# Kernel tuning notes

Hardware: AMD Instinct MI355X
Metric: run time of the kernel (lower is better)

## Reference

```python
import jax, jax.numpy as jnp
import numpy as np

BN_INV = 1.0 / np.float32(np.sqrt(1.0 + 1e-5))  # eval BN with running_mean=0, running_var=1


def _conv(x, w, stride):
    return jax.lax.conv_general_dilated(
        x, w, (stride, stride), [(1, 1), (1, 1)],
        dimension_numbers=('NCHW', 'OIHW', 'NCHW'))


def _se(x, w1, b1, w2, b2):
    # squeeze-excite: global avg pool -> fc -> relu -> fc -> sigmoid -> scale
    y = x.mean(axis=(2, 3))                       # (B, C)
    y = jax.nn.relu(y @ w1.T + b1)
    y = jax.nn.sigmoid(y @ w2.T + b2)
    return x * y[:, :, None, None]


def _squash(s):
    n2 = jnp.sum(s * s, axis=-1, keepdims=True)
    n = jnp.sqrt(n2)
    return s * (n2 / (1.0 + n2)) / (n + 1e-8)


def _block(x, cw, g, b, s1w, s1b, s2w, s2b, stride):
    h = _conv(x, cw, stride)
    h = h * (g * BN_INV)[None, :, None, None] + b[None, :, None, None]
    h = jax.nn.relu(h)
    return _se(h, s1w, s1b, s2w, s2b)


def setup_inputs() -> dict:
    key = jax.random.key(0)
    ks = jax.random.split(key, 32)
    rn = lambda i, shape, s=1.0: s * jax.random.normal(ks[i], shape, dtype=jnp.float32)
    d = {}
    d['x'] = rn(0, (64, 1, 128, 128))
    # feature extractor
    d['conv1_w'] = rn(1, (16, 1, 3, 3), 0.3)
    d['bn1_g'] = 1.0 + rn(2, (16,), 0.1)
    d['bn1_b'] = rn(3, (16,), 0.1)
    d['se1_w1'] = rn(4, (1, 16), 0.2); d['se1_b1'] = rn(5, (1,), 0.1)
    d['se1_w2'] = rn(6, (16, 1), 0.2); d['se1_b2'] = rn(7, (16,), 0.1)
    d['conv2_w'] = rn(8, (32, 16, 3, 3), 0.1)
    d['bn2_g'] = 1.0 + rn(9, (32,), 0.1)
    d['bn2_b'] = rn(10, (32,), 0.1)
    d['se2_w1'] = rn(11, (2, 32), 0.2); d['se2_b1'] = rn(12, (2,), 0.1)
    d['se2_w2'] = rn(13, (32, 2), 0.2); d['se2_b2'] = rn(14, (32,), 0.1)
    d['conv3_w'] = rn(15, (64, 32, 3, 3), 0.07)
    d['bn3_g'] = 1.0 + rn(16, (64,), 0.1)
    d['bn3_b'] = rn(17, (64,), 0.1)
    d['se3_w1'] = rn(18, (4, 64), 0.15); d['se3_b1'] = rn(19, (4,), 0.1)
    d['se3_w2'] = rn(20, (64, 4), 0.15); d['se3_b2'] = rn(21, (64,), 0.1)
    # primary capsules conv: 64 -> 8 caps * 8 dim = 64 channels, stride 2
    d['pc_w'] = rn(22, (64, 64, 3, 3), 0.05)
    d['pc_b'] = rn(23, (64,), 0.05)
    # digit capsule transform: (1, 2048, 3, 16, 8)
    d['W_digit'] = 0.01 * jax.random.normal(ks[24], (1, 2048, 3, 16, 8), dtype=jnp.float32)
    return d


def reference(x, conv1_w, bn1_g, bn1_b, se1_w1, se1_b1, se1_w2, se1_b2,
              conv2_w, bn2_g, bn2_b, se2_w1, se2_b1, se2_w2, se2_b2,
              conv3_w, bn3_g, bn3_b, se3_w1, se3_b1, se3_w2, se3_b2,
              pc_w, pc_b, W_digit):
    h = _block(x, conv1_w, bn1_g, bn1_b, se1_w1, se1_b1, se1_w2, se1_b2, 1)
    h = _block(h, conv2_w, bn2_g, bn2_b, se2_w1, se2_b1, se2_w2, se2_b2, 2)
    h = _block(h, conv3_w, bn3_g, bn3_b, se3_w1, se3_b1, se3_w2, se3_b2, 2)
    # primary capsules: conv -> (B, 8 caps, 8 dim, 16*16) -> (B, 2048, 8)
    u = _conv(h, pc_w, 2) + pc_b[None, :, None, None]     # (B, 64, 16, 16)
    B = u.shape[0]
    u = u.reshape(B, 8, 8, -1).transpose(0, 1, 3, 2).reshape(B, -1, 8)
    u = _squash(u)                                        # (B, 2048, 8)
    # u_hat[b,i,c,d] = sum_e W[0,i,c,d,e] * u[b,i,e]  (avoids torch's W.repeat)
    u_hat = jnp.einsum('icde,bie->bicd', W_digit[0], u)   # (B, 2048, 3, 16)
    b_ij = jnp.zeros((B, u_hat.shape[1], u_hat.shape[2], 1), u_hat.dtype)
    v_j = None
    for _ in range(3):  # fixed routing iterations
        c_ij = jax.nn.softmax(b_ij, axis=2)
        s_j = jnp.sum(c_ij * u_hat, axis=1, keepdims=True)  # (B,1,3,16)
        v_j = _squash(s_j)
        b_ij = b_ij + jnp.sum(u_hat * v_j, axis=-1, keepdims=True)
    v = v_j[:, 0]                                          # (B, 3, 16)
    return jnp.sqrt(jnp.sum(v * v, axis=-1))               # (B, 3) class lengths
```

## Files before the change

kernel.cpp:

```cpp
#include <hip/hip_runtime.h>
#include <math.h>

#define BN_INV_F 0.9999950000374997f

__device__ __forceinline__ void gload_lds4(const float* g, float* l) {
    __builtin_amdgcn_global_load_lds(
        (const __attribute__((address_space(1))) void*)g,
        (__attribute__((address_space(3))) void*)l, 4, 0, 0);
}
__device__ __forceinline__ void gload_lds16(const float* g, float* l) {
    __builtin_amdgcn_global_load_lds(
        (const __attribute__((address_space(1))) void*)g,
        (__attribute__((address_space(3))) void*)l, 16, 0, 0);
}

__global__ __launch_bounds__(256) void wtrans_all_k(
    const float* __restrict__ w1, const float* __restrict__ w2,
    const float* __restrict__ w3, const float* __restrict__ wp,
    float* __restrict__ w1t, float* __restrict__ w2t,
    float* __restrict__ w3t, float* __restrict__ wpt)
{
    int i = blockIdx.x * 256 + threadIdx.x;
    if (i < 144) {
        int co = i % 16, k = i / 16;
        w1t[i] = w1[co * 9 + k];
    } else if (i < 4752) {
        int t = i - 144;
        int co = t % 32, rk = t / 32, cin = rk / 9, k = rk % 9;
        w2t[t] = w2[(co * 16 + cin) * 9 + k];
    } else if (i < 23184) {
        int t = i - 4752;
        int co = t % 64, rk = t / 64, cin = rk / 9, k = rk % 9;
        w3t[t] = w3[(co * 32 + cin) * 9 + k];
    } else if (i < 60048) {
        int t = i - 23184;
        int co = t % 64, rk = t / 64, cin = rk / 9, k = rk % 9;
        wpt[t] = wp[(co * 64 + cin) * 9 + k];
    }
}

template <int CIN, int CINB, int COUT, int COB, int HIN, int HOUT, int STRIDE,
          int TW, int ROWS_T, int PPT, int CB, int NTHREADS,
          bool BN_RELU, bool SE_SUM, int HSE_IN, int KSPLIT>
__device__ __forceinline__ void conv_body(
    const float* __restrict__ in, const float* __restrict__ wt,
    const float* __restrict__ gamma, const float* __restrict__ beta,
    float* __restrict__ out, size_t pstride,
    float* __restrict__ se_sum, const float* __restrict__ se_sums_in,
    const float* __restrict__ se_w1, const float* __restrict__ se_b1,
    const float* __restrict__ se_w2, const float* __restrict__ se_b2,
    float inv_spatial)
{
    constexpr int WIN = HIN, WOUT = HOUT;
    constexpr int TH = ROWS_T * PPT;
    constexpr int IH_T = (TH - 1) * STRIDE + 3;
    constexpr int NW = NTHREADS / 64;
    constexpr int NCHUNK = CINB / CB;
    constexpr int SEGS = (WIN >= 64) ? (WIN / 64) : 1;
    constexpr int PAIRS = (IH_T + 1) / 2;
    constexpr int NG = COUT / COB;
    constexpr int IHW = IH_T * WIN;
    constexpr int CHUNK_BYTES = CB * IHW * 4;
    constexpr bool FAST16 = (CHUNK_BYTES % 1024) == 0;
    constexpr int NISS = CHUNK_BYTES / 1024;
    static_assert(NTHREADS == TW * ROWS_T, "geometry");
    static_assert(TW == WOUT, "tile must span full output width");
    static_assert(CINB % CB == 0, "chunking");
    static_assert(WIN % 64 == 0 || WIN == 32, "stage width");

    const int b = blockIdx.z;
    const int gy = blockIdx.y;
    const int ty = blockIdx.x;
    const int tid = threadIdx.x;
    const int wo = tid % TW;
    const int rg = tid / TW;
    const int g = gy % NG;
    const int kk = gy / NG;
    const int cin0 = kk * CINB;

    __shared__ float in_t[2][CB * IH_T * WIN];
    __shared__ float scl[CIN];
    __shared__ float gl[COB], bl[COB];
    __shared__ float red[NW][COB];
    __shared__ float hid[HSE_IN > 0 ? HSE_IN : 1];

    const float* inb = in + (size_t)b * CIN * HIN * WIN;
    const int gr0 = ty * TH * STRIDE - 1;
    const int wos = wo * STRIDE;
    const int wvid = tid >> 6, lane = tid & 63;
    const bool interior = (gr0 >= 0) && (gr0 + IH_T <= HIN);

    auto stage = [&](int c, int buf) {
        const int cb0 = cin0 + c * CB;
        float* bb = &in_t[buf][0];
        if (FAST16 && interior) {
            for (int i = wvid; i < NISS; i += NW) {
                int fe = i * 256 + lane * 4;
                int ci = fe / IHW;
                int rem = fe - ci * IHW;
                int lr = rem / WIN;
                int lc = rem - lr * WIN;
                const float* gsrc = inb + (size_t)(cb0 + ci) * (HIN * WIN)
                                  + (size_t)(gr0 + lr) * WIN + lc;
                gload_lds16(gsrc, bb + i * 256);
            }
        } else if (WIN >= 64) {
            for (int r = wvid; r < CB * IH_T; r += NW) {
                int ci = r / IH_T, lr = r - ci * IH_T;
                int gr = gr0 + lr;
                float* ldst = bb + (ci * IH_T + lr) * WIN;
                if (gr >= 0 && gr < HIN) {
                    const float* gsrc = inb + (size_t)(cb0 + ci) * HIN * WIN + (size_t)gr * WIN;
#pragma unroll
                    for (int s = 0; s < SEGS; ++s)
                        gload_lds4(gsrc + s * 64 + lane, ldst + s * 64);
                } else {
#pragma unroll
                    for (int s = 0; s < SEGS; ++s) ldst[s * 64 + lane] = 0.0f;
                }
            }
        } else {
            for (int pz = wvid; pz < CB * PAIRS; pz += NW) {
                int ci = pz / PAIRS, q = pz - ci * PAIRS;
                int lr0 = q * 2;
                int nr = (lr0 + 1 < IH_T) ? 2 : 1;
                int grr = gr0 + lr0;
                float* ldst = bb + (ci * IH_T + lr0) * WIN;
                if (nr == 2 && grr >= 0 && grr + 1 < HIN) {
                    const float* gsrc = inb + (size_t)(cb0 + ci) * HIN * WIN + (size_t)grr * WIN + lane;
                    gload_lds4(gsrc, ldst);
                } else {
                    for (int e = lane; e < nr * WIN; e += 64) {
                        int rr = e / WIN, cc = e - rr * WIN;
                        int gr = grr + rr;
                        ldst[e] = (gr >= 0 && gr < HIN)
                            ? inb[(size_t)(cb0 + ci) * HIN * WIN + (size_t)gr * WIN + cc] : 0.0f;
                    }
                }
            }
        }
    };

    stage(0, 0);

    if (HSE_IN > 0) {
        if (tid < HSE_IN) {
            float a = se_b1[tid];
            for (int c = 0; c < CIN; ++c)
                a = fmaf(se_sums_in[b * CIN + c] * inv_spatial, se_w1[tid * CIN + c], a);
            hid[tid] = fmaxf(a, 0.0f);
        }
        __syncthreads();
        if (tid < CIN) {
            float a = se_b2[tid];
            for (int h = 0; h < HSE_IN; ++h)
                a = fmaf(hid[h], se_w2[tid * HSE_IN + h], a);
            scl[tid] = 1.0f / (1.0f + expf(-a));
        }
    } else {
        for (int t = tid; t < CIN; t += NTHREADS) scl[t] = 1.0f;
    }
    if (tid < COB) {
        int co = g * COB + tid;
        if (BN_RELU) {
            gl[tid] = gamma[co] * BN_INV_F;
            bl[tid] = beta[co];
        } else {
            gl[tid] = (kk == 0) ? gamma[co] : 0.0f;
        }
    }

    float acc[PPT][COB];
#pragma unroll
    for (int p = 0; p < PPT; ++p)
#pragma unroll
        for (int co = 0; co < COB; ++co) acc[p][co] = 0.0f;

    int cur = 0;
    for (int c = 0; c < NCHUNK; ++c) {
        asm volatile("s_waitcnt vmcnt(0)" ::: "memory");
        __syncthreads();
        if (c + 1 < NCHUNK) stage(c + 1, cur ^ 1);

        const float* bb = &in_t[cur][0];
#pragma unroll
        for (int ci = 0; ci < CB; ++ci) {
            const int cw = cin0 + c * CB + ci;
            const float sc = scl[cw];
            const float* wtap = wt + (size_t)cw * 9 * COUT + g * COB;
            const float* bb_ci = bb + ci * IH_T * WIN;

            float iw[PPT][3][3];
#pragma unroll
            for (int p = 0; p < PPT; ++p) {
                const int r0 = (rg + p * ROWS_T) * STRIDE;
#pragma unroll
                for (int kh = 0; kh < 3; ++kh) {
                    const float* row = bb_ci + (r0 + kh) * WIN;
#pragma unroll
                    for (int kw = 0; kw < 3; ++kw) {
                        int wi = wos + kw - 1;
                        float v;
                        if (kw == 0) {
                            v = row[wi < 0 ? 0 : wi];
                            if (wi < 0) v = 0.0f;
                        } else if (STRIDE == 1 && kw == 2) {
                            v = row[wi >= WIN ? WIN - 1 : wi];
                            if (wi >= WIN) v = 0.0f;
                        } else {
                            v = row[wi];
                        }
                        iw[p][kh][kw] = v * sc;
                    }
                }
            }

#pragma unroll
            for (int kh = 0; kh < 3; ++kh) {
#pragma unroll
                for (int kw = 0; kw < 3; ++kw) {
                    const float* wrow = wtap + (kh * 3 + kw) * COUT;
#pragma unroll
                    for (int p = 0; p < PPT; ++p) {
                        const float v = iw[p][kh][kw];
#pragma unroll
                        for (int co = 0; co < COB; ++co)
                            acc[p][co] = fmaf(wrow[co], v, acc[p][co]);
                    }
                }
            }
        }
        cur ^= 1;
    }

    float tsum[COB];
#pragma unroll
    for (int co = 0; co < COB; ++co) tsum[co] = 0.0f;
    float* ob = out + (size_t)kk * pstride
              + ((size_t)b * COUT + (size_t)g * COB) * HOUT * WOUT;
#pragma unroll
    for (int p = 0; p < PPT; ++p) {
        const int ho = ty * TH + rg + p * ROWS_T;
#pragma unroll
        for (int co = 0; co < COB; ++co) {
            float v;
            if (BN_RELU)
                v = fmaxf(fmaf(acc[p][co], gl[co], bl[co]), 0.0f);
            else
                v = acc[p][co] + gl[co];
            ob[(size_t)co * HOUT * WOUT + ho * WOUT + wo] = v;
            tsum[co] += v;
        }
    }

    if (SE_SUM) {
#pragma unroll
        for (int co = 0; co < COB; ++co) {
            float v = tsum[co];
            for (int off = 32; off; off >>= 1) v += __shfl_down(v, off, 64);
            if (lane == 0) red[wvid][co] = v;
        }
        __syncthreads();
        if (tid < COB) {
            float v = 0.0f;
#pragma unroll
            for (int k = 0; k < NW; ++k) v += red[k][tid];
            atomicAdd(&se_sum[b * COUT + g * COB + tid], v);
        }
    }
}

#define CONV_ARGS \
    const float* __restrict__ in, const float* __restrict__ wt, \
    const float* __restrict__ gamma, const float* __restrict__ beta, \
    float* __restrict__ out, size_t pstride, float* __restrict__ se_sum, \
    const float* __restrict__ se_sums_in, \
    const float* __restrict__ se_w1, const float* __restrict__ se_b1, \
    const float* __restrict__ se_w2, const float* __restrict__ se_b2, \
    float inv_spatial
#define CONV_PASS in, wt, gamma, beta, out, pstride, se_sum, se_sums_in, \
    se_w1, se_b1, se_w2, se_b2, inv_spatial

__global__ __launch_bounds__(256) void conv1_k(CONV_ARGS) {
    conv_body<1, 1, 16, 16, 128, 128, 1, 128, 2, 2, 1, 256, true, true, 0, 1>(CONV_PASS);
}
__global__ __launch_bounds__(256) void conv2_k(CONV_ARGS) {
    conv_body<16, 16, 32, 32, 128, 64, 2, 64, 4, 1, 4, 256, true, true, 1, 1>(CONV_PASS);
}
__global__ __launch_bounds__(256) void conv3_k(CONV_ARGS) {
    conv_body<32, 16, 64, 32, 64, 32, 2, 32, 8, 1, 4, 256, false, false, 2, 2>(CONV_PASS);
}
__global__ __launch_bounds__(256) void pc_k(CONV_ARGS) {
    conv_body<64, 16, 64, 16, 32, 16, 2, 16, 16, 1, 4, 256, false, false, 4, 4>(CONV_PASS);
}

__global__ __launch_bounds__(256) void cb_k(const float* __restrict__ pA,
                                            const float* __restrict__ pB,
                                            const float* __restrict__ gamma,
                                            const float* __restrict__ beta,
                                            float* __restrict__ h3,
                                            float* __restrict__ s3)
{
    const int bc = blockIdx.x;
    const int c = bc & 63;
    const int tid = threadIdx.x;
    __shared__ float red[4];
    const size_t base = (size_t)bc * 1024;
    float4 a = ((const float4*)(pA + base))[tid];
    float4 d = ((const float4*)(pB + base))[tid];
    const float g = gamma[c] * BN_INV_F, be = beta[c];
    float4 v;
    v.x = fmaxf(fmaf(a.x + d.x, g, be), 0.0f);
    v.y = fmaxf(fmaf(a.y + d.y, g, be), 0.0f);
    v.z = fmaxf(fmaf(a.z + d.z, g, be), 0.0f);
    v.w = fmaxf(fmaf(a.w + d.w, g, be), 0.0f);
    ((float4*)(h3 + base))[tid] = v;
    float s = (v.x + v.y) + (v.z + v.w);
    for (int off = 32; off; off >>= 1) s += __shfl_down(s, off, 64);
    const int lane = tid & 63, wv = tid >> 6;
    if (lane == 0) red[wv] = s;
    __syncthreads();
    if (tid == 0) s3[bc] = (red[0] + red[1]) + (red[2] + red[3]);
}

__global__ __launch_bounds__(256) void squash_uhat_k(
    const float* __restrict__ up, size_t pstride,
    const float* __restrict__ W, float* __restrict__ u_hat)
{
    const int base = blockIdx.x * 256;
    const int tid = threadIdx.x;
    __shared__ float ush[256][8];

    {
        const int cap = base + tid;
        const int b = cap >> 11, i = cap & 2047;
        const int chi = i >> 8, spx = i & 255;
        const size_t off = ((size_t)(b * 64 + chi * 8)) * 256 + spx;
        float s[8];
        float n2 = 0.0f;
#pragma unroll
        for (int j = 0; j < 8; j++) {
            const size_t o = off + (size_t)j * 256;
            s[j] = (up[o] + up[o + pstride]) + (up[o + 2 * pstride] + up[o + 3 * pstride]);
            n2 = fmaf(s[j], s[j], n2);
        }
        const float n = sqrtf(n2);
        const float f = (n2 / (1.0f + n2)) / (n + 1e-8f);
#pragma unroll
        for (int j = 0; j < 8; j++) ush[tid][j] = s[j] * f;
    }
    __syncthreads();

    float* ob = u_hat + (size_t)base * 48;
#pragma unroll 4
    for (int k = 0; k < 48; ++k) {
        int o = tid + k * 256;
        int c = o / 48, cd = o % 48;
        int gi = (base + c) & 2047;
        const float* wp = W + (size_t)gi * 384 + cd * 8;
        float a = 0.0f;
#pragma unroll
        for (int e = 0; e < 8; e++) a = fmaf(wp[e], ush[c][e], a);
        ob[o] = a;
    }
}

template <int IT>
__global__ __launch_bounds__(256) void sweep_k(const float* __restrict__ u_hat,
                                               const float* __restrict__ s_hist,
                                               float* __restrict__ s_out)
{
    const int b = blockIdx.y;
    const int i = blockIdx.x * 256 + threadIdx.x;
    const int tid = threadIdx.x;
    __shared__ float vsh[IT > 0 ? IT : 1][48];
    __shared__ float fac[IT > 0 ? IT : 1][3];
    __shared__ float red[4][48];

    const float4* qp = (const float4*)(u_hat + ((size_t)b * 2048 + i) * 48);
    float uhv[48];
#pragma unroll
    for (int q = 0; q < 12; ++q) {
        float4 t = qp[q];
        uhv[q * 4 + 0] = t.x; uhv[q * 4 + 1] = t.y;
        uhv[q * 4 + 2] = t.z; uhv[q * 4 + 3] = t.w;
    }

    if (IT > 0) {
        if (tid < IT * 48) {
            int t = tid / 48, c = tid % 48;
            vsh[t][c] = s_hist[((size_t)t * 64 + b) * 48 + c];
        }
        __syncthreads();
        if (tid < IT * 3) {
            int t = tid / 3, j = tid % 3;
            float n2 = 0.0f;
            for (int d = 0; d < 16; ++d) { float s = vsh[t][j * 16 + d]; n2 = fmaf(s, s, n2); }
            float n = sqrtf(n2);
            fac[t][j] = (n2 / (1.0f + n2)) / (n + 1e-8f);
        }
        __syncthreads();
        if (tid < IT * 48) {
            int t = tid / 48, c = tid % 48;
            vsh[t][c] *= fac[t][c / 16];
        }
        __syncthreads();
    }

    float c0, c1, c2;
    if (IT == 0) {
        c0 = c1 = c2 = (1.0f / 3.0f);
    } else {
        float b0 = 0.0f, b1 = 0.0f, b2 = 0.0f;
#pragma unroll
        for (int t = 0; t < IT; ++t)
#pragma unroll
            for (int d = 0; d < 16; ++d) {
                b0 = fmaf(uhv[d],      vsh[t][d],      b0);
                b1 = fmaf(uhv[16 + d], vsh[t][16 + d], b1);
                b2 = fmaf(uhv[32 + d], vsh[t][32 + d], b2);
            }
        float m = fmaxf(b0, fmaxf(b1, b2));
        float e0 = expf(b0 - m), e1 = expf(b1 - m), e2 = expf(b2 - m);
        float inv = 1.0f / (e0 + e1 + e2);
        c0 = e0 * inv; c1 = e1 * inv; c2 = e2 * inv;
    }

    float sp[48];
#pragma unroll
    for (int d = 0; d < 16; ++d) {
        sp[d]      = c0 * uhv[d];
        sp[16 + d] = c1 * uhv[16 + d];
        sp[32 + d] = c2 * uhv[32 + d];
    }
    const int lane = tid & 63, wv = tid >> 6;
#pragma unroll
    for (int j = 0; j < 48; ++j) {
        float x = sp[j];
        for (int off = 32; off; off >>= 1) x += __shfl_down(x, off, 64);
        if (lane == 0) red[wv][j] = x;
    }
    __syncthreads();
    if (tid < 48) {
        float x = red[0][tid] + red[1][tid] + red[2][tid] + red[3][tid];
        atomicAdd(&s_out[(size_t)b * 48 + tid], x);
    }
}

__global__ __launch_bounds__(64) void route_out_k(const float* __restrict__ s2,
                                                  float* __restrict__ out)
{
    const int b = blockIdx.x;
    __shared__ float s[48];
    if (threadIdx.x < 48) s[threadIdx.x] = s2[(size_t)b * 48 + threadIdx.x];
    __syncthreads();
    if (threadIdx.x < 3) {
        int j = threadIdx.x;
        float n2 = 0.0f;
        for (int d = 0; d < 16; ++d) { float v = s[j * 16 + d]; n2 = fmaf(v, v, n2); }
        float n = sqrtf(n2);
        float fc = (n2 / (1.0f + n2)) / (n + 1e-8f);
        out[b * 3 + j] = fc * n;
    }
}

extern "C" void kernel_launch(void* const* d_in, const int* in_sizes, int n_in,
                              void* d_out, int out_size, void* d_ws, size_t ws_size,
                              hipStream_t stream)
{
    const float* x       = (const float*)d_in[0];
    const float* conv1_w = (const float*)d_in[1];
    const float* bn1_g   = (const float*)d_in[2];
    const float* bn1_b   = (const float*)d_in[3];
    const float* se1_w1  = (const float*)d_in[4];
    const float* se1_b1  = (const float*)d_in[5];
    const float* se1_w2  = (const float*)d_in[6];
    const float* se1_b2  = (const float*)d_in[7];
    const float* conv2_w = (const float*)d_in[8];
    const float* bn2_g   = (const float*)d_in[9];
    const float* bn2_b   = (const float*)d_in[10];
    const float* se2_w1  = (const float*)d_in[11];
    const float* se2_b1  = (const float*)d_in[12];
    const float* se2_w2  = (const float*)d_in[13];
    const float* se2_b2  = (const float*)d_in[14];
    const float* conv3_w = (const float*)d_in[15];
    const float* bn3_g   = (const float*)d_in[16];
    const float* bn3_b   = (const float*)d_in[17];
    const float* se3_w1  = (const float*)d_in[18];
    const float* se3_b1  = (const float*)d_in[19];
    const float* se3_w2  = (const float*)d_in[20];
    const float* se3_b2  = (const float*)d_in[21];
    const float* pc_w    = (const float*)d_in[22];
    const float* pc_b    = (const float*)d_in[23];
    const float* W_digit = (const float*)d_in[24];

    float* ws = (float*)d_ws;
    float* h1     = ws;
    float* h2     = ws + 16777216;
    float* h3     = ws;
    float* cp0    = ws + 4194304;
    float* cp1    = ws + 8388608;
    float* uparts = ws + 4194304;
    float* u_hat  = ws + 9437184;
    float* sums   = ws + 25165824;
    float* s1 = sums, *s2 = sums + 1024, *s3 = sums + 3072;
    float* s_buf  = sums + 7168;
    float* zeros64 = sums + 16384;
    float* w1t    = ws + 25182272;
    float* w2t    = w1t + 144;
    float* w3t    = w2t + 4608;
    float* wpt    = w3t + 18432;

    hipMemsetAsync(sums, 0, 16448 * sizeof(float), stream);
    wtrans_all_k<<<235, 256, 0, stream>>>(conv1_w, conv2_w, conv3_w, pc_w,
                                          w1t, w2t, w3t, wpt);

    conv1_k<<<dim3(32, 1, 64), 256, 0, stream>>>(
        x, w1t, bn1_g, bn1_b, h1, 0, s1,
        nullptr, nullptr, nullptr, nullptr, nullptr, 0.0f);

    conv2_k<<<dim3(16, 1, 64), 256, 0, stream>>>(
        h1, w2t, bn2_g, bn2_b, h2, 0, s2,
        s1, se1_w1, se1_b1, se1_w2, se1_b2, 1.0f / 16384.0f);

    conv3_k<<<dim3(4, 4, 64), 256, 0, stream>>>(
        h2, w3t, zeros64, nullptr, cp0, (size_t)4194304, nullptr,
        s2, se2_w1, se2_b1, se2_w2, se2_b2, 1.0f / 4096.0f);

    cb_k<<<4096, 256, 0, stream>>>(cp0, cp1, bn3_g, bn3_b, h3, s3);

    pc_k<<<dim3(1, 16, 64), 256, 0, stream>>>(
        h3, wpt, pc_b, nullptr, uparts, (size_t)1048576, nullptr,
        s3, se3_w1, se3_b1, se3_w2, se3_b2, 1.0f / 1024.0f);

    squash_uhat_k<<<512, 256, 0, stream>>>(uparts, (size_t)1048576, W_digit, u_hat);

    sweep_k<0><<<dim3(8, 64), 256, 0, stream>>>(u_hat, s_buf, s_buf + 0 * 64 * 48);
    sweep_k<1><<<dim3(8, 64), 256, 0, stream>>>(u_hat, s_buf, s_buf + 1 * 64 * 48);
    sweep_k<2><<<dim3(8, 64), 256, 0, stream>>>(u_hat, s_buf, s_buf + 2 * 64 * 48);
    route_out_k<<<64, 64, 0, stream>>>(s_buf + 2 * 64 * 48, (float*)d_out);
}
```

Baseline: 227.9 us.

## Add wave-split conv kernel for conv2/conv3 and fuse BN/SE into conv3

Adds a new conv body in which each wave computes its own slice of output channels (WCO per wave), so wave-uniform weight addresses can come from scalar loads, and the whole tile spans the full output width. conv2 and conv3 switch to this body. conv3 drops its K-split, handling all 32 input channels in one 512-thread block and applying BN+ReLU and the SE sum directly, which removes the partial-sum buffers and the separate combine kernel. The existing conv body also interleaves the input reads with the FMAs instead of first buffering all taps, to lower register pressure. In exchange, conv3 launches fewer blocks and its per-block work is more serialized.

New measurement: 224.5 us. No clear change (-1.5%).

```diff
diff --git a/kernel.cpp b/kernel.cpp
--- a/kernel.cpp
+++ b/kernel.cpp
@@ -189,16 +189,14 @@
             const float sc = scl[cw];
             const float* wtap = wt + (size_t)cw * 9 * COUT + g * COB;
             const float* bb_ci = bb + ci * IH_T * WIN;
-
-            float iw[PPT][3][3];
-#pragma unroll
-            for (int p = 0; p < PPT; ++p) {
-                const int r0 = (rg + p * ROWS_T) * STRIDE;
-#pragma unroll
-                for (int kh = 0; kh < 3; ++kh) {
-                    const float* row = bb_ci + (r0 + kh) * WIN;
-#pragma unroll
-                    for (int kw = 0; kw < 3; ++kw) {
+#pragma unroll
+            for (int kh = 0; kh < 3; ++kh) {
+#pragma unroll
+                for (int kw = 0; kw < 3; ++kw) {
+                    const float* wrow = wtap + (kh * 3 + kw) * COUT;
+#pragma unroll
+                    for (int p = 0; p < PPT; ++p) {
+                        const float* row = bb_ci + ((rg + p * ROWS_T) * STRIDE + kh) * WIN;
                         int wi = wos + kw - 1;
                         float v;
                         if (kw == 0) {
@@ -210,19 +208,7 @@
                         } else {
                             v = row[wi];
                         }
-                        iw[p][kh][kw] = v * sc;
-                    }
-                }
-            }
-
-#pragma unroll
-            for (int kh = 0; kh < 3; ++kh) {
-#pragma unroll
-                for (int kw = 0; kw < 3; ++kw) {
-                    const float* wrow = wtap + (kh * 3 + kw) * COUT;
-#pragma unroll
-                    for (int p = 0; p < PPT; ++p) {
-                        const float v = iw[p][kh][kw];
+                        v *= sc;
 #pragma unroll
                         for (int co = 0; co < COB; ++co)
                             acc[p][co] = fmaf(wrow[co], v, acc[p][co]);
@@ -267,6 +253,222 @@
             for (int k = 0; k < NW; ++k) v += red[k][tid];
             atomicAdd(&se_sum[b * COUT + g * COB + tid], v);
         }
+    }
+}
+
+template <int CIN, int CINB, int COUT, int WCO, int HIN, int HOUT, int STRIDE,
+          int TW, int PPT, int CB, int NTHREADS,
+          bool BN_RELU, bool SE_SUM, int HSE_IN, int KSPLIT>
+__device__ __forceinline__ void conv_ws_body(
+    const float* __restrict__ in, const float* __restrict__ wt,
+    const float* __restrict__ gamma, const float* __restrict__ beta,
+    float* __restrict__ out, size_t pstride,
+    float* __restrict__ se_sum, const float* __restrict__ se_sums_in,
+    const float* __restrict__ se_w1, const float* __restrict__ se_b1,
+    const float* __restrict__ se_w2, const float* __restrict__ se_b2,
+    float inv_spatial)
+{
+    constexpr int WIN = HIN, WOUT = HOUT;
+    constexpr int NW = NTHREADS / 64;
+    constexpr int WROWS = 64 / TW;
+    constexpr int TH = WROWS * PPT;
+    constexpr int IH_T = (TH - 1) * STRIDE + 3;
+    constexpr int COBT = NW * WCO;
+    constexpr int NG = COUT / COBT;
+    constexpr int NCHUNK = CINB / CB;
+    constexpr int SEGS = (WIN >= 64) ? (WIN / 64) : 1;
+    constexpr int PAIRS = (IH_T + 1) / 2;
+    constexpr int IHW = IH_T * WIN;
+    constexpr int CHUNK_BYTES = CB * IHW * 4;
+    constexpr bool FAST16 = (CHUNK_BYTES % 1024) == 0;
+    constexpr int NISS = CHUNK_BYTES / 1024;
+    static_assert(TW == WOUT, "tile spans full width");
+    static_assert(CINB % CB == 0, "chunking");
+    static_assert(WIN % 64 == 0 || WIN == 32, "stage width");
+    static_assert(COUT % COBT == 0, "cout split");
+
+    const int b = blockIdx.z;
+    const int gy = blockIdx.y;
+    const int ty = blockIdx.x;
+    const int tid = threadIdx.x;
+    const int lane = tid & 63;
+    const int wvu = __builtin_amdgcn_readfirstlane(tid >> 6);
+    const int wo = lane % TW;
+    const int rl = lane / TW;
+    const int g = gy % NG;
+    const int kk = gy / NG;
+    const int cin0 = kk * CINB;
+
+    __shared__ float in_t[2][CB * IH_T * WIN];
+    __shared__ float scl[CIN];
+    __shared__ float gl[COBT], bl[COBT];
+    __shared__ float red[NW][WCO];
+    __shared__ float hid[HSE_IN > 0 ? HSE_IN : 1];
+
+    const float* inb = in + (size_t)b * CIN * HIN * WIN;
+    const int gr0 = ty * TH * STRIDE - 1;
+    const int wos = wo * STRIDE;
+    const bool interior = (gr0 >= 0) && (gr0 + IH_T <= HIN);
+
+    auto stage = [&](int c, int buf) {
+        const int cb0 = cin0 + c * CB;
+        float* bb = &in_t[buf][0];
+        if (FAST16 && interior) {
+            for (int i = wvu; i < NISS; i += NW) {
+                int fe = i * 256 + lane * 4;
+                int ci = fe / IHW;
+                int rem = fe - ci * IHW;
+                int lr = rem / WIN;
+                int lc = rem - lr * WIN;
+                const float* gsrc = inb + (size_t)(cb0 + ci) * (HIN * WIN)
+                                  + (size_t)(gr0 + lr) * WIN + lc;
+                gload_lds16(gsrc, bb + i * 256);
+            }
+        } else if (WIN >= 64) {
+            for (int r = wvu; r < CB * IH_T; r += NW) {
+                int ci = r / IH_T, lr = r - ci * IH_T;
+                int gr = gr0 + lr;
+                float* ldst = bb + (ci * IH_T + lr) * WIN;
+                if (gr >= 0 && gr < HIN) {
+                    const float* gsrc = inb + (size_t)(cb0 + ci) * HIN * WIN + (size_t)gr * WIN;
+#pragma unroll
+                    for (int s = 0; s < SEGS; ++s)
+                        gload_lds4(gsrc + s * 64 + lane, ldst + s * 64);
+                } else {
+#pragma unroll
+                    for (int s = 0; s < SEGS; ++s) ldst[s * 64 + lane] = 0.0f;
+                }
+            }
+        } else {
+            for (int pz = wvu; pz < CB * PAIRS; pz += NW) {
+                int ci = pz / PAIRS, q = pz - ci * PAIRS;
+                int lr0 = q * 2;
+                int nr = (lr0 + 1 < IH_T) ? 2 : 1;
+                int grr = gr0 + lr0;
+                float* ldst = bb + (ci * IH_T + lr0) * WIN;
+                if (nr == 2 && grr >= 0 && grr + 1 < HIN) {
+                    const float* gsrc = inb + (size_t)(cb0 + ci) * HIN * WIN + (size_t)grr * WIN + lane;
+                    gload_lds4(gsrc, ldst);
+                } else {
+                    for (int e = lane; e < nr * WIN; e += 64) {
+                        int rr = e / WIN, cc = e - rr * WIN;
+                        int gr = grr + rr;
+                        ldst[e] = (gr >= 0 && gr < HIN)
+                            ? inb[(size_t)(cb0 + ci) * HIN * WIN + (size_t)gr * WIN + cc] : 0.0f;
+                    }
+                }
+            }
+        }
+    };
+
+    stage(0, 0);
+
+    if (HSE_IN > 0) {
+        if (tid < HSE_IN) {
+            float a = se_b1[tid];
+            for (int c = 0; c < CIN; ++c)
+                a = fmaf(se_sums_in[b * CIN + c] * inv_spatial, se_w1[tid * CIN + c], a);
+            hid[tid] = fmaxf(a, 0.0f);
+        }
+        __syncthreads();
+        if (tid < CIN) {
+            float a = se_b2[tid];
+            for (int h = 0; h < HSE_IN; ++h)
+                a = fmaf(hid[h], se_w2[tid * HSE_IN + h], a);
+            scl[tid] = 1.0f / (1.0f + expf(-a));
+        }
+    } else {
+        for (int t = tid; t < CIN; t += NTHREADS) scl[t] = 1.0f;
+    }
+    if (tid < COBT) {
+        int co = g * COBT + tid;
+        if (BN_RELU) {
+            gl[tid] = gamma[co] * BN_INV_F;
+            bl[tid] = beta[co];
+        } else {
+            gl[tid] = (kk == 0) ? gamma[co] : 0.0f;
+        }
+    }
+
+    float acc[PPT][WCO];
+#pragma unroll
+    for (int p = 0; p < PPT; ++p)
+#pragma unroll
+        for (int co = 0; co < WCO; ++co) acc[p][co] = 0.0f;
+
+    int cur = 0;
+    for (int c = 0; c < NCHUNK; ++c) {
+        asm volatile("s_waitcnt vmcnt(0)" ::: "memory");
+        __syncthreads();
+        if (c + 1 < NCHUNK) stage(c + 1, cur ^ 1);
+
+        const float* bb = &in_t[cur][0];
+#pragma unroll
+        for (int ci = 0; ci < CB; ++ci) {
+            const int cw = cin0 + c * CB + ci;
+            const float sc = scl[cw];
+            const float* wtap = wt + (size_t)cw * 9 * COUT + g * COBT + wvu * WCO;
+            const float* bb_ci = bb + ci * IH_T * WIN;
+#pragma unroll
+            for (int kh = 0; kh < 3; ++kh) {
+#pragma unroll
+                for (int kw = 0; kw < 3; ++kw) {
+                    const float* wrow = wtap + (kh * 3 + kw) * COUT;
+#pragma unroll
+                    for (int p = 0; p < PPT; ++p) {
+                        const float* row = bb_ci + ((rl + p * WROWS) * STRIDE + kh) * WIN;
+                        int wi = wos + kw - 1;
+                        float v;
+                        if (kw == 0) {
+                            v = row[wi < 0 ? 0 : wi];
+                            if (wi < 0) v = 0.0f;
+                        } else if (STRIDE == 1 && kw == 2) {
+                            v = row[wi >= WIN ? WIN - 1 : wi];
+                            if (wi >= WIN) v = 0.0f;
+                        } else {
+                            v = row[wi];
+                        }
+                        v *= sc;
+#pragma unroll
+                        for (int co = 0; co < WCO; ++co)
+                            acc[p][co] = fmaf(wrow[co], v, acc[p][co]);
+                    }
+                }
+            }
+        }
+        cur ^= 1;
+    }
+
+    float tsum[WCO];
+#pragma unroll
+    for (int co = 0; co < WCO; ++co) tsum[co] = 0.0f;
+    float* ob = out + (size_t)kk * pstride
+              + ((size_t)b * COUT + (size_t)g * COBT + (size_t)wvu * WCO) * HOUT * WOUT;
+#pragma unroll
+    for (int p = 0; p < PPT; ++p) {
+        const int ho = ty * TH + rl + p * WROWS;
+#pragma unroll
+        for (int co = 0; co < WCO; ++co) {
+            float v;
+            if (BN_RELU)
+                v = fmaxf(fmaf(acc[p][co], gl[wvu * WCO + co], bl[wvu * WCO + co]), 0.0f);
+            else
+                v = acc[p][co] + gl[wvu * WCO + co];
+            ob[(size_t)co * HOUT * WOUT + ho * WOUT + wo] = v;
+            tsum[co] += v;
+        }
+    }
+
+    if (SE_SUM) {
+#pragma unroll
+        for (int co = 0; co < WCO; ++co) {
+            float v = tsum[co];
+            for (int off = 32; off; off >>= 1) v += __shfl_down(v, off, 64);
+            if (lane == 0) red[wvu][co] = v;
+        }
+        __syncthreads();
+        if (lane < WCO)
+            atomicAdd(&se_sum[b * COUT + g * COBT + wvu * WCO + lane], red[wvu][lane]);
     }
 }
 
@@ -285,42 +487,13 @@
     conv_body<1, 1, 16, 16, 128, 128, 1, 128, 2, 2, 1, 256, true, true, 0, 1>(CONV_PASS);
 }
 __global__ __launch_bounds__(256) void conv2_k(CONV_ARGS) {
-    conv_body<16, 16, 32, 32, 128, 64, 2, 64, 4, 1, 4, 256, true, true, 1, 1>(CONV_PASS);
-}
-__global__ __launch_bounds__(256) void conv3_k(CONV_ARGS) {
-    conv_body<32, 16, 64, 32, 64, 32, 2, 32, 8, 1, 4, 256, false, false, 2, 2>(CONV_PASS);
+    conv_ws_body<16, 16, 32, 8, 128, 64, 2, 64, 4, 4, 256, true, true, 1, 1>(CONV_PASS);
+}
+__global__ __launch_bounds__(512) void conv3_k(CONV_ARGS) {
+    conv_ws_body<32, 32, 64, 8, 64, 32, 2, 32, 2, 8, 512, true, true, 2, 1>(CONV_PASS);
 }
 __global__ __launch_bounds__(256) void pc_k(CONV_ARGS) {
     conv_body<64, 16, 64, 16, 32, 16, 2, 16, 16, 1, 4, 256, false, false, 4, 4>(CONV_PASS);
-}
-
-__global__ __launch_bounds__(256) void cb_k(const float* __restrict__ pA,
-                                            const float* __restrict__ pB,
-                                            const float* __restrict__ gamma,
-                                            const float* __restrict__ beta,
-                                            float* __restrict__ h3,
-                                            float* __restrict__ s3)
-{
-    const int bc = blockIdx.x;
-    const int c = bc & 63;
-    const int tid = threadIdx.x;
-    __shared__ float red[4];
-    const size_t base = (size_t)bc * 1024;
-    float4 a = ((const float4*)(pA + base))[tid];
-    float4 d = ((const float4*)(pB + base))[tid];
-    const float g = gamma[c] * BN_INV_F, be = beta[c];
-    float4 v;
-    v.x = fmaxf(fmaf(a.x + d.x, g, be), 0.0f);
-    v.y = fmaxf(fmaf(a.y + d.y, g, be), 0.0f);
-    v.z = fmaxf(fmaf(a.z + d.z, g, be), 0.0f);
-    v.w = fmaxf(fmaf(a.w + d.w, g, be), 0.0f);
-    ((float4*)(h3 + base))[tid] = v;
-    float s = (v.x + v.y) + (v.z + v.w);
-    for (int off = 32; off; off >>= 1) s += __shfl_down(s, off, 64);
-    const int lane = tid & 63, wv = tid >> 6;
-    if (lane == 0) red[wv] = s;
-    __syncthreads();
-    if (tid == 0) s3[bc] = (red[0] + red[1]) + (red[2] + red[3]);
 }
 
 __global__ __launch_bounds__(256) void squash_uhat_k(
@@ -498,14 +671,11 @@
     float* h1     = ws;
     float* h2     = ws + 16777216;
     float* h3     = ws;
-    float* cp0    = ws + 4194304;
-    float* cp1    = ws + 8388608;
     float* uparts = ws + 4194304;
     float* u_hat  = ws + 9437184;
     float* sums   = ws + 25165824;
     float* s1 = sums, *s2 = sums + 1024, *s3 = sums + 3072;
     float* s_buf  = sums + 7168;
-    float* zeros64 = sums + 16384;
     float* w1t    = ws + 25182272;
     float* w2t    = w1t + 144;
     float* w3t    = w2t + 4608;
@@ -523,11 +693,9 @@
         h1, w2t, bn2_g, bn2_b, h2, 0, s2,
         s1, se1_w1, se1_b1, se1_w2, se1_b2, 1.0f / 16384.0f);
 
-    conv3_k<<<dim3(4, 4, 64), 256, 0, stream>>>(
-        h2, w3t, zeros64, nullptr, cp0, (size_t)4194304, nullptr,
+    conv3_k<<<dim3(8, 1, 64), 512, 0, stream>>>(
+        h2, w3t, bn3_g, bn3_b, h3, 0, s3,
         s2, se2_w1, se2_b1, se2_w2, se2_b2, 1.0f / 4096.0f);
-
-    cb_k<<<4096, 256, 0, stream>>>(cp0, cp1, bn3_g, bn3_b, h3, s3);
 
     pc_k<<<dim3(1, 16, 64), 256, 0, stream>>>(
         h3, wpt, pc_b, nullptr, uparts, (size_t)1048576, nullptr,
```
